# Optimization experiments

Measured on AMD Instinct MI355X. Metric: run time of the kernel, lower is better.

Reference implementation:

```python
import jax, jax.numpy as jnp
import numpy as np

B, T, D_MODEL, STATE = 4, 4096, 1024, 256
LN_EPS = 1e-5


def setup_inputs() -> dict:
    key = jax.random.key(0)
    ks = jax.random.split(key, 8)
    x = jax.random.normal(ks[0], (B, T, D_MODEL), dtype=jnp.float32)
    bound_d = 1.0 / np.sqrt(D_MODEL)
    bound_n = 1.0 / np.sqrt(STATE)
    Wa_w = jax.random.normal(ks[1], (STATE, D_MODEL), dtype=jnp.float32) * 0.02
    Wa_b = jnp.zeros((STATE,), dtype=jnp.float32)
    WB_w = jax.random.normal(ks[2], (STATE, D_MODEL), dtype=jnp.float32) * 0.02
    WB_b = jax.random.uniform(ks[3], (STATE,), jnp.float32, -bound_d, bound_d)
    WC_w = jax.random.normal(ks[4], (D_MODEL, STATE), dtype=jnp.float32) * 0.02
    WC_b = jax.random.uniform(ks[5], (D_MODEL,), jnp.float32, -bound_n, bound_n)
    log_gamma = jnp.asarray(0.0, dtype=jnp.float32)
    D_skip = jax.random.normal(ks[6], (D_MODEL,), dtype=jnp.float32) * 0.01
    ln_w = jnp.ones((D_MODEL,), dtype=jnp.float32)
    ln_b = jnp.zeros((D_MODEL,), dtype=jnp.float32)
    return {"x": x, "Wa_w": Wa_w, "Wa_b": Wa_b, "log_gamma": log_gamma,
            "WB_w": WB_w, "WB_b": WB_b, "WC_w": WC_w, "WC_b": WC_b,
            "D_skip": D_skip, "ln_w": ln_w, "ln_b": ln_b}


def _layernorm(x, w, b):
    mu = jnp.mean(x, axis=-1, keepdims=True)
    var = jnp.mean(jnp.square(x - mu), axis=-1, keepdims=True)
    return (x - mu) * jax.lax.rsqrt(var + LN_EPS) * w + b


def reference(x, Wa_w, Wa_b, log_gamma, WB_w, WB_b, WC_w, WC_b, D_skip, ln_w, ln_b):
    residual = x
    xn = _layernorm(x, ln_w, ln_b)                      # (B,T,D)
    # Fourier eigenvalues: gamma * tanh(W_a x), FFT, magnitude-contracting scale
    gamma = jax.nn.sigmoid(log_gamma)
    a = gamma * jnp.tanh(jnp.einsum('btd,nd->btn', xn, Wa_w) + Wa_b)  # (B,T,n) real
    a_hat = jnp.fft.fft(a, axis=-1)                     # (B,T,n) complex, conj-symmetric
    mag = jnp.maximum(jnp.abs(a_hat), 1e-8)
    a_hat = a_hat * jax.nn.sigmoid(2.0 * (1.0 - mag))
    # Input projection in Fourier domain
    u = jnp.einsum('btd,nd->btn', xn, WB_w) + WB_b
    u_hat = jnp.fft.fft(u, axis=-1)                     # (B,T,n) complex
    # Linear recurrence h_t = a_t * h_{t-1} + b_t via associative scan over time
    def combine(c1, c2):
        a1, b1 = c1
        a2, b2 = c2
        return (a1 * a2, a2 * b1 + b2)
    _, h_hat = jax.lax.associative_scan(combine, (a_hat, u_hat), axis=1)
    h = jnp.real(jnp.fft.ifft(h_hat, axis=-1)).astype(x.dtype)        # (B,T,n)
    y = jnp.einsum('btn,dn->btd', h, WC_w) + WC_b + D_skip * residual
    return y
```

## Files before the change

kernel.cpp:

```cpp
#include <hip/hip_runtime.h>


typedef unsigned short ushort_t;
typedef short s16x8 __attribute__((ext_vector_type(8)));
typedef float f32x4 __attribute__((ext_vector_type(4)));
typedef _Float16 f16x8 __attribute__((ext_vector_type(8)));
typedef _Float16 f16x2 __attribute__((ext_vector_type(2)));

#define B_ 4
#define T_ 4096
#define D_ 1024
#define N_ 256
#define KB_ 129
#define M_ (B_*T_)

#define SWZ(i) ((i) ^ (((i) >> 3) & 6))

__device__ __forceinline__ ushort_t f2bf(float f) {
  unsigned u = __float_as_uint(f);
  u = (u + 0x7FFFu + ((u >> 16) & 1u)) >> 16;
  return (ushort_t)u;
}
__device__ __forceinline__ float2 cmul(float2 a, float2 b) {
  return make_float2(a.x*b.x - a.y*b.y, a.x*b.y + a.y*b.x);
}
__device__ __forceinline__ float fast_tanh(float x) {
  return 1.f - 2.f / (__expf(2.f * x) + 1.f);
}

typedef const __attribute__((address_space(1))) unsigned glb_u32;
typedef __attribute__((address_space(3))) unsigned lds_u32;
__device__ __forceinline__ void gload16(const void* g, void* l) {
  __builtin_amdgcn_global_load_lds((glb_u32*)g, (lds_u32*)l, 16, 0, 0);
}

__global__ __launch_bounds__(256) void ln_prep_kernel(const float* __restrict__ x,
    const float* __restrict__ w, const float* __restrict__ bb,
    ushort_t* __restrict__ xn,
    const float* __restrict__ Wa, const float* __restrict__ WB,
    const float* __restrict__ WC, ushort_t* __restrict__ Wab,
    ushort_t* __restrict__ WCb) {
  int tid = threadIdx.x;
  if (blockIdx.x >= 4096) {
    int i4 = ((blockIdx.x - 4096) * 256 + tid) * 4;
    float4 v;
    ushort_t* dst;
    if (i4 < 262144)        { v = *(const float4*)(Wa + i4);          dst = Wab + i4; }
    else if (i4 < 524288)   { v = *(const float4*)(WB + i4 - 262144); dst = Wab + i4; }
    else                    { v = *(const float4*)(WC + i4 - 524288); dst = WCb + i4 - 524288; }
    ushort4 o;
    o.x = f2bf(v.x); o.y = f2bf(v.y); o.z = f2bf(v.z); o.w = f2bf(v.w);
    *(ushort4*)dst = o;
    return;
  }
  int lane = tid & 63, wv = tid >> 6;
  int row = blockIdx.x * 4 + wv;
  const float4* xr = (const float4*)(x + (size_t)row * D_);
  float4 v[4];
  float s = 0.f, sq = 0.f;
  #pragma unroll
  for (int j = 0; j < 4; ++j) {
    v[j] = xr[lane + 64 * j];
    s  += v[j].x + v[j].y + v[j].z + v[j].w;
    sq += v[j].x*v[j].x + v[j].y*v[j].y + v[j].z*v[j].z + v[j].w*v[j].w;
  }
  #pragma unroll
  for (int off = 32; off >= 1; off >>= 1) {
    s  += __shfl_xor(s, off);
    sq += __shfl_xor(sq, off);
  }
  float mu  = s * (1.0f / D_);
  float var = sq * (1.0f / D_) - mu * mu;
  float rs  = rsqrtf(var + 1e-5f);
  const float4* w4 = (const float4*)w;
  const float4* b4 = (const float4*)bb;
  ushort4* o4 = (ushort4*)(xn + (size_t)row * D_);
  #pragma unroll
  for (int j = 0; j < 4; ++j) {
    float4 wv_ = w4[lane + 64 * j];
    float4 bv_ = b4[lane + 64 * j];
    ushort4 o;
    o.x = f2bf((v[j].x - mu) * rs * wv_.x + bv_.x);
    o.y = f2bf((v[j].y - mu) * rs * wv_.y + bv_.y);
    o.z = f2bf((v[j].z - mu) * rs * wv_.z + bv_.z);
    o.w = f2bf((v[j].w - mu) * rs * wv_.w + bv_.w);
    o4[lane + 64 * j] = o;
  }
}

template<bool EPI, int BN, bool HOUT>
__global__ __launch_bounds__(256) void gemm_bf16(
    const ushort_t* __restrict__ A, int lda,
    const ushort_t* __restrict__ B, int ldb,
    void* __restrict__ Cv, int ldc,
    int K, int ntiles,
    const float* __restrict__ bias,
    const float* __restrict__ dskip,
    const float* __restrict__ xres) {
  constexpr int NF = BN / 32;
  __shared__ ushort_t Alds[128 * 64];
  __shared__ ushort_t Blds[BN * 64];
  int bid = blockIdx.x;
  int cpx = gridDim.x >> 3;
  bid = (bid & 7) * cpx + (bid >> 3);
  int mt = bid / ntiles, nt = bid % ntiles;
  int m0 = mt * 128, n0 = nt * BN;
  int tid = threadIdx.x;
  int lane = tid & 63, wid = tid >> 6;
  int wm = wid >> 1, wn = wid & 1;

  int lr8 = lane >> 3;
  int gd  = (lane & 7) ^ lr8;
  const ushort_t* gA = A + (size_t)(m0 + wid * 32 + lr8) * lda + gd * 8;
  ushort_t* lA = &Alds[(wid * 32) * 64];
  constexpr int BROWS = BN / 4;
  const ushort_t* gB = B + (size_t)(n0 + wid * BROWS + lr8) * ldb + gd * 8;
  ushort_t* lB = &Blds[(wid * BROWS) * 64];

  f32x4 acc[4][NF] = {};
  int rbase = lane & 15;
  int rb7 = lane & 7;
  int gk0 = lane >> 4;

  for (int k0 = 0; k0 < K; k0 += 64) {
    __syncthreads();
    #pragma unroll
    for (int c = 0; c < 4; ++c)
      gload16(gA + (size_t)(c * 8) * lda + k0, lA + c * 8 * 64);
    #pragma unroll
    for (int c = 0; c < BROWS / 8; ++c)
      gload16(gB + (size_t)(c * 8) * ldb + k0, lB + c * 8 * 64);
    __syncthreads();
    #pragma unroll
    for (int kk = 0; kk < 2; ++kk) {
      int sl = ((gk0 + kk * 4) ^ rb7) * 8;
      s16x8 af[4], bf[NF];
      #pragma unroll
      for (int i = 0; i < 4; ++i)
        af[i] = *reinterpret_cast<const s16x8*>(&Alds[(wm * 64 + i * 16 + rbase) * 64 + sl]);
      #pragma unroll
      for (int j = 0; j < NF; ++j)
        bf[j] = *reinterpret_cast<const s16x8*>(&Blds[(wn * (BN / 2) + j * 16 + rbase) * 64 + sl]);
      #pragma unroll
      for (int i = 0; i < 4; ++i)
        #pragma unroll
        for (int j = 0; j < NF; ++j)
          acc[i][j] = __builtin_amdgcn_mfma_f32_16x16x32_bf16(af[i], bf[j], acc[i][j], 0, 0, 0);
    }
  }

  int r0 = (lane >> 4) * 4, cc = lane & 15;
  #pragma unroll
  for (int i = 0; i < 4; ++i) {
    #pragma unroll
    for (int j = 0; j < NF; ++j) {
      int col = n0 + wn * (BN / 2) + j * 16 + cc;
      #pragma unroll
      for (int r = 0; r < 4; ++r) {
        int row = m0 + wm * 64 + i * 16 + r0 + r;
        float v = acc[i][j][r];
        if constexpr (EPI) v += bias[col] + dskip[col] * xres[(size_t)row * ldc + col];
        if constexpr (HOUT) ((_Float16*)Cv)[(size_t)row * ldc + col] = (_Float16)v;
        else                ((float*)Cv)[(size_t)row * ldc + col] = v;
      }
    }
  }
}

__global__ __launch_bounds__(512) void fft_fwd(const _Float16* __restrict__ au,
    const float* __restrict__ ba, const float* __restrict__ bu,
    const float* __restrict__ lg, _Float16* __restrict__ ah, _Float16* __restrict__ uh) {
  __shared__ float2 Z[8][256];
  __shared__ float2 Tw[128];
  int tid = threadIdx.x;
  int m0 = blockIdx.x * 8;
  int tg = tid >> 6, lane = tid & 63;
  if (tid < 128) {
    float sn, cs;
    __sincosf(-3.14159265358979f / 128.f * (float)tid, &sn, &cs);
    Tw[SWZ(tid)] = make_float2(cs, sn);
  }
  float gamma = 1.f / (1.f + __expf(-lg[0]));
  const _Float16* row = au + (size_t)(m0 + tg) * (2 * N_);
  #pragma unroll
  for (int j = 0; j < 4; ++j) {
    int n = lane + 64 * j;
    float a = gamma * fast_tanh((float)row[n] + ba[n]);
    float u = (float)row[N_ + n] + bu[n];
    Z[tg][SWZ(__brev((unsigned)n) >> 24)] = make_float2(a, u);
  }
  __syncthreads();
  #pragma unroll
  for (int st = 1; st <= 8; ++st) {
    int half = 1 << (st - 1), shift = 8 - st;
    #pragma unroll
    for (int s = 0; s < 2; ++s) {
      int bi = lane + 64 * s;
      int j = bi & (half - 1);
      int i0 = ((bi & ~(half - 1)) << 1) | j;
      int i1 = i0 + half;
      float2 tw = Tw[SWZ(j << shift)];
      float2 z0 = Z[tg][SWZ(i0)], z1 = Z[tg][SWZ(i1)];
      float2 t = cmul(tw, z1);
      Z[tg][SWZ(i1)] = make_float2(z0.x - t.x, z0.y - t.y);
      Z[tg][SWZ(i0)] = make_float2(z0.x + t.x, z0.y + t.y);
    }
    __syncthreads();
  }
  int b = m0 >> 12, tb = m0 & (T_ - 1);
  #pragma unroll
  for (int p = 0; p < 3; ++p) {
    int k = (tid >> 3) + p * 64;
    int tl = tid & 7;
    if (k <= 128) {
      float2 zk = Z[tl][SWZ(k)];
      float2 zn = Z[tl][SWZ((256 - k) & 255)];
      float2 Af = make_float2(0.5f * (zk.x + zn.x), 0.5f * (zk.y - zn.y));
      float2 Uf = make_float2(0.5f * (zk.y + zn.y), -0.5f * (zk.x - zn.x));
      float mag = fmaxf(sqrtf(Af.x * Af.x + Af.y * Af.y), 1e-8f);
      float scl = 1.f / (1.f + __expf(-2.f * (1.f - mag)));
      Af.x *= scl; Af.y *= scl;
      size_t off2 = (((size_t)(b * KB_ + k)) * T_ + tb + tl) * 2;
      f16x2 av; av[0] = (_Float16)Af.x; av[1] = (_Float16)Af.y;
      f16x2 uv; uv[0] = (_Float16)Uf.x; uv[1] = (_Float16)Uf.y;
      *(f16x2*)(ah + off2) = av;
      *(f16x2*)(uh + off2) = uv;
    }
  }
}

__global__ __launch_bounds__(512) void scan_kernel(const _Float16* __restrict__ ah,
                                                   _Float16* __restrict__ uh) {
  __shared__ float4 wagg[8];
  int tid = threadIdx.x;
  int lane = tid & 63, wv = tid >> 6;
  size_t base = (size_t)blockIdx.x * T_ * 2;
  const f16x8* a8 = (const f16x8*)(ah + base);
  f16x8* u8 = (f16x8*)(uh + base);
  f16x8 Av[2], Uv[2];
  #pragma unroll
  for (int q = 0; q < 2; ++q) { Av[q] = a8[tid * 2 + q]; Uv[q] = u8[tid * 2 + q]; }
  float2 La[8], Lb[8];
  float2 ra = make_float2(1.f, 0.f), rb = make_float2(0.f, 0.f);
  #pragma unroll
  for (int e = 0; e < 8; ++e) {
    const int q = e >> 2, i = (e & 3) * 2;
    float2 a = make_float2((float)Av[q][i], (float)Av[q][i + 1]);
    float2 u = make_float2((float)Uv[q][i], (float)Uv[q][i + 1]);
    float2 t = cmul(a, rb);
    rb = make_float2(t.x + u.x, t.y + u.y);
    ra = cmul(ra, a);
    La[e] = ra; Lb[e] = rb;
  }
  #pragma unroll
  for (int off = 1; off < 64; off <<= 1) {
    float ax = __shfl_up(ra.x, off, 64), ay = __shfl_up(ra.y, off, 64);
    float bx = __shfl_up(rb.x, off, 64), by = __shfl_up(rb.y, off, 64);
    if (lane >= off) {
      float2 Ap = make_float2(ax, ay), Bp = make_float2(bx, by);
      float2 nB = cmul(ra, Bp);
      nB.x += rb.x; nB.y += rb.y;
      ra = cmul(Ap, ra);
      rb = nB;
    }
  }
  if (lane == 63) wagg[wv] = make_float4(ra.x, ra.y, rb.x, rb.y);
  __syncthreads();
  float2 Bw = make_float2(0.f, 0.f);
  for (int w0 = 0; w0 < wv; ++w0) {
    float4 g = wagg[w0];
    float2 gA = make_float2(g.x, g.y), gB = make_float2(g.z, g.w);
    Bw = cmul(gA, Bw);
    Bw.x += gB.x; Bw.y += gB.y;
  }
  float ax = __shfl_up(ra.x, 1, 64), ay = __shfl_up(ra.y, 1, 64);
  float bx = __shfl_up(rb.x, 1, 64), by = __shfl_up(rb.y, 1, 64);
  float2 Ae, Be;
  if (lane == 0) { Ae = make_float2(1.f, 0.f); Be = make_float2(0.f, 0.f); }
  else           { Ae = make_float2(ax, ay);   Be = make_float2(bx, by);   }
  float2 Pb = cmul(Ae, Bw);
  Pb.x += Be.x; Pb.y += Be.y;
  #pragma unroll
  for (int q = 0; q < 2; ++q) {
    f16x8 o;
    #pragma unroll
    for (int e2 = 0; e2 < 4; ++e2) {
      const int e = q * 4 + e2;
      float2 h = cmul(La[e], Pb);
      h.x += Lb[e].x; h.y += Lb[e].y;
      o[e2 * 2]     = (_Float16)h.x;
      o[e2 * 2 + 1] = (_Float16)h.y;
    }
    u8[tid * 2 + q] = o;
  }
}

__global__ __launch_bounds__(256) void ifft_kernel(const _Float16* __restrict__ hh,
                                                   ushort_t* __restrict__ hb) {
  __shared__ float2 Hraw[8][132];
  __shared__ float2 Wz[4][256];
  __shared__ float2 Tw[128];
  int tid = threadIdx.x;
  int m0 = blockIdx.x * 8;
  int b = m0 >> 12, tb = m0 & (T_ - 1);
  if (tid < 128) {
    float sn, cs;
    __sincosf(3.14159265358979f / 128.f * (float)tid, &sn, &cs);
    Tw[SWZ(tid)] = make_float2(cs, sn);
  }
  #pragma unroll
  for (int p = 0; p < 5; ++p) {
    int k = p * 32 + (tid >> 3), tl = tid & 7;
    if (k <= 128) {
      f16x2 hv = *(const f16x2*)(hh + (((size_t)(b * KB_ + k)) * T_ + tb + tl) * 2);
      Hraw[tl][k] = make_float2((float)hv[0], (float)hv[1]);
    }
  }
  __syncthreads();
  #pragma unroll
  for (int p = 0; p < 3; ++p) {
    int idx = p * 256 + tid;
    if (idx < 516) {
      int k = idx >> 2, pr = idx & 3;
      float2 h1 = Hraw[2 * pr][k], h2 = Hraw[2 * pr + 1][k];
      Wz[pr][SWZ(__brev((unsigned)k) >> 24)] = make_float2(h1.x - h2.y, h1.y + h2.x);
      if (k >= 1 && k <= 127)
        Wz[pr][SWZ(__brev((unsigned)(256 - k)) >> 24)] = make_float2(h1.x + h2.y, h2.x - h1.y);
    }
  }
  __syncthreads();
  int pr = tid >> 6, lane = tid & 63;
  #pragma unroll
  for (int st = 1; st <= 8; ++st) {
    int half = 1 << (st - 1), shift = 8 - st;
    #pragma unroll
    for (int s = 0; s < 2; ++s) {
      int bi = lane + 64 * s;
      int j = bi & (half - 1);
      int i0 = ((bi & ~(half - 1)) << 1) | j;
      int i1 = i0 + half;
      float2 tw = Tw[SWZ(j << shift)];
      float2 z0 = Wz[pr][SWZ(i0)], z1 = Wz[pr][SWZ(i1)];
      float2 t = cmul(tw, z1);
      Wz[pr][SWZ(i1)] = make_float2(z0.x - t.x, z0.y - t.y);
      Wz[pr][SWZ(i0)] = make_float2(z0.x + t.x, z0.y + t.y);
    }
    __syncthreads();
  }
  const float inv = 1.f / 256.f;
  #pragma unroll
  for (int j = 0; j < 4; ++j) {
    int n = lane + 64 * j;
    float2 wv = Wz[pr][SWZ(n)];
    hb[(size_t)(m0 + 2 * pr) * N_ + n]     = f2bf(wv.x * inv);
    hb[(size_t)(m0 + 2 * pr + 1) * N_ + n] = f2bf(wv.y * inv);
  }
}

extern "C" void kernel_launch(void* const* d_in, const int* in_sizes, int n_in,
                              void* d_out, int out_size, void* d_ws, size_t ws_size,
                              hipStream_t stream) {
  const float* x      = (const float*)d_in[0];
  const float* Wa_w   = (const float*)d_in[1];
  const float* Wa_b   = (const float*)d_in[2];
  const float* lg     = (const float*)d_in[3];
  const float* WB_w   = (const float*)d_in[4];
  const float* WB_b   = (const float*)d_in[5];
  const float* WC_w   = (const float*)d_in[6];
  const float* WC_b   = (const float*)d_in[7];
  const float* D_skip = (const float*)d_in[8];
  const float* ln_w   = (const float*)d_in[9];
  const float* ln_b   = (const float*)d_in[10];
  float* out = (float*)d_out;
  char* ws = (char*)d_ws;

  ushort_t*  xn  = (ushort_t*)(ws + 0);
  ushort_t*  Wab = (ushort_t*)(ws + 33554432);
  ushort_t*  WCb = (ushort_t*)(ws + 34603008);
  _Float16*  au  = (_Float16*)(ws + 35127296);
  ushort_t*  hb  = (ushort_t*)(ws + 35127296);
  _Float16*  ah  = (_Float16*)(ws + 0);
  _Float16*  uh  = (_Float16*)(ws + 16908288);

  ln_prep_kernel<<<4864, 256, 0, stream>>>(x, ln_w, ln_b, xn,
                                           Wa_w, WB_w, WC_w, Wab, WCb);
  gemm_bf16<false, 64, true><<<1024, 256, 0, stream>>>(xn, D_, Wab, D_, au, 512,
                                                       D_, 8, nullptr, nullptr, nullptr);
  fft_fwd<<<M_ / 8, 512, 0, stream>>>(au, Wa_b, WB_b, lg, ah, uh);
  scan_kernel<<<B_ * KB_, 512, 0, stream>>>(ah, uh);
  ifft_kernel<<<M_ / 8, 256, 0, stream>>>(uh, hb);
  gemm_bf16<true, 128, false><<<1024, 256, 0, stream>>>(hb, N_, WCb, N_, out, D_,
                                                        N_, 8, WC_b, D_skip, x);
}
```

Measured before the change: 113.3 us.

## Switch FFT butterflies to radix-4 with wave-local stages and no barriers

Replaces the 8-stage radix-2 FFT in the forward and inverse FFT kernels with a 4-stage radix-4 FFT, using base-4 digit-reversal input ordering and a full 256-entry twiddle table. Each 256-point transform is owned by a single 64-lane wavefront, so the per-stage __syncthreads are removed. This is meant to cut LDS traffic, barriers and index math per transform. It relies on wavefront lockstep ordering of LDS accesses, and the twiddle table takes more shared memory.

```diff
diff --git a/kernel.cpp b/kernel.cpp
--- a/kernel.cpp
+++ b/kernel.cpp
@@ -15,6 +15,7 @@
 #define M_ (B_*T_)
 
 #define SWZ(i) ((i) ^ (((i) >> 3) & 6))
+#define DR4(n) ((((n) & 3) << 6) | (((n) & 12) << 2) | (((n) & 48) >> 2) | (((n) >> 6) & 3))
 
 __device__ __forceinline__ ushort_t f2bf(float f) {
   unsigned u = __float_as_uint(f);
@@ -171,14 +172,14 @@
     const float* __restrict__ ba, const float* __restrict__ bu,
     const float* __restrict__ lg, _Float16* __restrict__ ah, _Float16* __restrict__ uh) {
   __shared__ float2 Z[8][256];
-  __shared__ float2 Tw[128];
+  __shared__ float2 Tw[256];
   int tid = threadIdx.x;
   int m0 = blockIdx.x * 8;
   int tg = tid >> 6, lane = tid & 63;
-  if (tid < 128) {
+  if (tid < 256) {
     float sn, cs;
-    __sincosf(-3.14159265358979f / 128.f * (float)tid, &sn, &cs);
-    Tw[SWZ(tid)] = make_float2(cs, sn);
+    __sincosf(-6.2831853071795864f / 256.f * (float)tid, &sn, &cs);
+    Tw[tid] = make_float2(cs, sn);
   }
   float gamma = 1.f / (1.f + __expf(-lg[0]));
   const _Float16* row = au + (size_t)(m0 + tg) * (2 * N_);
@@ -187,26 +188,37 @@
     int n = lane + 64 * j;
     float a = gamma * fast_tanh((float)row[n] + ba[n]);
     float u = (float)row[N_ + n] + bu[n];
-    Z[tg][SWZ(__brev((unsigned)n) >> 24)] = make_float2(a, u);
+    Z[tg][SWZ(DR4(n))] = make_float2(a, u);
   }
   __syncthreads();
   #pragma unroll
-  for (int st = 1; st <= 8; ++st) {
-    int half = 1 << (st - 1), shift = 8 - st;
-    #pragma unroll
-    for (int s = 0; s < 2; ++s) {
-      int bi = lane + 64 * s;
-      int j = bi & (half - 1);
-      int i0 = ((bi & ~(half - 1)) << 1) | j;
-      int i1 = i0 + half;
-      float2 tw = Tw[SWZ(j << shift)];
-      float2 z0 = Z[tg][SWZ(i0)], z1 = Z[tg][SWZ(i1)];
-      float2 t = cmul(tw, z1);
-      Z[tg][SWZ(i1)] = make_float2(z0.x - t.x, z0.y - t.y);
-      Z[tg][SWZ(i0)] = make_float2(z0.x + t.x, z0.y + t.y);
-    }
-    __syncthreads();
-  }
+  for (int ls = 0; ls < 4; ++ls) {
+    const int Q = 1 << (2 * ls);
+    const int step = 64 >> (2 * ls);
+    int j = lane & (Q - 1);
+    int g = lane >> (2 * ls);
+    int base = g * (4 * Q) + j;
+    float2 a0 = Z[tg][SWZ(base)];
+    float2 a1 = Z[tg][SWZ(base + Q)];
+    float2 a2 = Z[tg][SWZ(base + 2 * Q)];
+    float2 a3 = Z[tg][SWZ(base + 3 * Q)];
+    if (ls > 0) {
+      int e = j * step;
+      a1 = cmul(a1, Tw[e]);
+      a2 = cmul(a2, Tw[2 * e]);
+      a3 = cmul(a3, Tw[3 * e]);
+    }
+    float2 t0 = make_float2(a0.x + a2.x, a0.y + a2.y);
+    float2 t1 = make_float2(a0.x - a2.x, a0.y - a2.y);
+    float2 t2 = make_float2(a1.x + a3.x, a1.y + a3.y);
+    float2 d  = make_float2(a1.x - a3.x, a1.y - a3.y);
+    float2 t3 = make_float2(d.y, -d.x);
+    Z[tg][SWZ(base)]         = make_float2(t0.x + t2.x, t0.y + t2.y);
+    Z[tg][SWZ(base + Q)]     = make_float2(t1.x + t3.x, t1.y + t3.y);
+    Z[tg][SWZ(base + 2 * Q)] = make_float2(t0.x - t2.x, t0.y - t2.y);
+    Z[tg][SWZ(base + 3 * Q)] = make_float2(t1.x - t3.x, t1.y - t3.y);
+  }
+  __syncthreads();
   int b = m0 >> 12, tb = m0 & (T_ - 1);
   #pragma unroll
   for (int p = 0; p < 3; ++p) {
@@ -299,14 +311,14 @@
                                                    ushort_t* __restrict__ hb) {
   __shared__ float2 Hraw[8][132];
   __shared__ float2 Wz[4][256];
-  __shared__ float2 Tw[128];
+  __shared__ float2 Tw[256];
   int tid = threadIdx.x;
   int m0 = blockIdx.x * 8;
   int b = m0 >> 12, tb = m0 & (T_ - 1);
-  if (tid < 128) {
+  {
     float sn, cs;
-    __sincosf(3.14159265358979f / 128.f * (float)tid, &sn, &cs);
-    Tw[SWZ(tid)] = make_float2(cs, sn);
+    __sincosf(6.2831853071795864f / 256.f * (float)tid, &sn, &cs);
+    Tw[tid] = make_float2(cs, sn);
   }
   #pragma unroll
   for (int p = 0; p < 5; ++p) {
@@ -323,29 +335,39 @@
     if (idx < 516) {
       int k = idx >> 2, pr = idx & 3;
       float2 h1 = Hraw[2 * pr][k], h2 = Hraw[2 * pr + 1][k];
-      Wz[pr][SWZ(__brev((unsigned)k) >> 24)] = make_float2(h1.x - h2.y, h1.y + h2.x);
+      Wz[pr][SWZ(DR4(k))] = make_float2(h1.x - h2.y, h1.y + h2.x);
       if (k >= 1 && k <= 127)
-        Wz[pr][SWZ(__brev((unsigned)(256 - k)) >> 24)] = make_float2(h1.x + h2.y, h2.x - h1.y);
+        Wz[pr][SWZ(DR4(256 - k))] = make_float2(h1.x + h2.y, h2.x - h1.y);
     }
   }
   __syncthreads();
   int pr = tid >> 6, lane = tid & 63;
   #pragma unroll
-  for (int st = 1; st <= 8; ++st) {
-    int half = 1 << (st - 1), shift = 8 - st;
-    #pragma unroll
-    for (int s = 0; s < 2; ++s) {
-      int bi = lane + 64 * s;
-      int j = bi & (half - 1);
-      int i0 = ((bi & ~(half - 1)) << 1) | j;
-      int i1 = i0 + half;
-      float2 tw = Tw[SWZ(j << shift)];
-      float2 z0 = Wz[pr][SWZ(i0)], z1 = Wz[pr][SWZ(i1)];
-      float2 t = cmul(tw, z1);
-      Wz[pr][SWZ(i1)] = make_float2(z0.x - t.x, z0.y - t.y);
-      Wz[pr][SWZ(i0)] = make_float2(z0.x + t.x, z0.y + t.y);
-    }
-    __syncthreads();
+  for (int ls = 0; ls < 4; ++ls) {
+    const int Q = 1 << (2 * ls);
+    const int step = 64 >> (2 * ls);
+    int j = lane & (Q - 1);
+    int g = lane >> (2 * ls);
+    int base = g * (4 * Q) + j;
+    float2 a0 = Wz[pr][SWZ(base)];
+    float2 a1 = Wz[pr][SWZ(base + Q)];
+    float2 a2 = Wz[pr][SWZ(base + 2 * Q)];
+    float2 a3 = Wz[pr][SWZ(base + 3 * Q)];
+    if (ls > 0) {
+      int e = j * step;
+      a1 = cmul(a1, Tw[e]);
+      a2 = cmul(a2, Tw[2 * e]);
+      a3 = cmul(a3, Tw[3 * e]);
+    }
+    float2 t0 = make_float2(a0.x + a2.x, a0.y + a2.y);
+    float2 t1 = make_float2(a0.x - a2.x, a0.y - a2.y);
+    float2 t2 = make_float2(a1.x + a3.x, a1.y + a3.y);
+    float2 d  = make_float2(a1.x - a3.x, a1.y - a3.y);
+    float2 t3 = make_float2(-d.y, d.x);
+    Wz[pr][SWZ(base)]         = make_float2(t0.x + t2.x, t0.y + t2.y);
+    Wz[pr][SWZ(base + Q)]     = make_float2(t1.x + t3.x, t1.y + t3.y);
+    Wz[pr][SWZ(base + 2 * Q)] = make_float2(t0.x - t2.x, t0.y - t2.y);
+    Wz[pr][SWZ(base + 3 * Q)] = make_float2(t1.x - t3.x, t1.y - t3.y);
   }
   const float inv = 1.f / 256.f;
   #pragma unroll
```

After: 108.1 us. 4.6% less time.
